# Performance work log

Measured on AMD Instinct MI355X. Metric: run time of the kernel, lower is better.

Reference implementation:

```python
import jax, jax.numpy as jnp
import numpy as np


def setup_inputs() -> dict:
    key = jax.random.key(0)
    k1, k2, k3 = jax.random.split(key, 3)
    B, C, H, W = 16, 256, 48, 48
    INTER = C // 2
    x = jax.random.normal(k1, (B, C, H, W), dtype=jnp.float32)
    # nn.init.normal_(weight, std=0.01); 1x1 conv kernels stored as (out, in)
    theta_w = 0.01 * jax.random.normal(k2, (INTER, C), dtype=jnp.float32)
    phi_w = 0.01 * jax.random.normal(k3, (INTER, C), dtype=jnp.float32)
    theta_b = jnp.zeros((INTER,), dtype=jnp.float32)
    phi_b = jnp.zeros((INTER,), dtype=jnp.float32)
    return {"x": x, "theta_w": theta_w, "theta_b": theta_b, "phi_w": phi_w, "phi_b": phi_b}


def reference(x, theta_w, theta_b, phi_w, phi_b):
    b, c, h, w = x.shape
    inter = theta_w.shape[0]
    n = h * w
    # 1x1 conv == channel-wise linear projection
    theta_x = jnp.einsum('bchw,kc->bkhw', x, theta_w) + theta_b[None, :, None, None]
    phi_x = jnp.einsum('bchw,kc->bkhw', x, phi_w) + phi_b[None, :, None, None]
    q = theta_x.reshape(b, inter, n)   # [b, k, n]
    kmat = phi_x.reshape(b, inter, n)  # [b, k, n]
    g = x.reshape(b, c, n)             # [b, c, n]
    # f = theta^T @ phi : [b, n, n], scaled then softmaxed over last dim
    f = jnp.einsum('bkn,bkm->bnm', q, kmat) / jnp.sqrt(jnp.asarray(inter, x.dtype))
    f = jax.nn.softmax(f, axis=-1)
    # y = f @ g^T : [b, c, n]
    y = jnp.einsum('bnm,bcm->bcn', f, g)
    return y.reshape(b, c, h, w)
```

## Files before the change

### kernel.cpp

```cpp
#include <hip/hip_runtime.h>
#include <hip/hip_bf16.h>

#define B_SZ 16
#define C_IN 256
#define N_SP 2304
#define K_INT 128
#define NTILE 36
#define MT 32
#define MITER 72

typedef __attribute__((ext_vector_type(8))) short short8;
typedef __attribute__((ext_vector_type(4))) float f32x4;

__device__ inline unsigned pk_bf16(float a, float b) {
  float2 f; f.x = a; f.y = b;
  __hip_bfloat162 h = __float22bfloat162_rn(f);
  unsigned u;
  __builtin_memcpy(&u, &h, sizeof(u));
  return u;
}

__device__ inline short8 ldw_bf16(const float* __restrict__ W, int k, int c0) {
  const float* wp = W + (size_t)k * C_IN + c0;
  float4 w0 = ((const float4*)wp)[0];
  float4 w1 = ((const float4*)wp)[1];
  unsigned u[4];
  u[0] = pk_bf16(w0.x, w0.y); u[1] = pk_bf16(w0.z, w0.w);
  u[2] = pk_bf16(w1.x, w1.y); u[3] = pk_bf16(w1.z, w1.w);
  short8 a;
  __builtin_memcpy(&a, u, sizeof(a));
  return a;
}

__global__ __launch_bounds__(256) void proj_kernel(
    const float* __restrict__ x,
    const float* __restrict__ theta_w, const float* __restrict__ theta_b,
    const float* __restrict__ phi_w,   const float* __restrict__ phi_b,
    short* __restrict__ Qt, short* __restrict__ Kt, short* __restrict__ Gbf)
{
  __shared__ __align__(16) char Xs[32768];

  const int b  = blockIdx.x / NTILE;
  const int n0 = (blockIdx.x % NTILE) * 64;
  const int t  = threadIdx.x;
  const int wave = t >> 6, lane = t & 63;
  const int col = lane & 15, quad = lane >> 4;

  {
    const int tq = t >> 4;
    const int a  = t & 15;
    const float* xs = x + ((size_t)b * C_IN + tq * 4) * N_SP + n0 + a * 4;
    short* gs = Gbf + ((size_t)b * C_IN + tq * 4) * N_SP + n0 + a * 4;
#pragma unroll
    for (int s = 0; s < 4; ++s) {
      unsigned us[4][2];
#pragma unroll
      for (int r = 0; r < 4; ++r) {
        float4 v = *(const float4*)(xs + ((size_t)s * 64 + r) * N_SP);
        us[r][0] = pk_bf16(v.x, v.y);
        us[r][1] = pk_bf16(v.z, v.w);
        uint2 u; u.x = us[r][0]; u.y = us[r][1];
        *(uint2*)(gs + ((size_t)s * 64 + r) * N_SP) = u;
      }
      const int chunk = 8 * s + (tq >> 1);
      const int half8 = (tq & 1) * 8;
#pragma unroll
      for (int j = 0; j < 4; ++j) {
        const int w = j >> 1;
        unsigned w0, w1;
        if ((j & 1) == 0) {
          w0 = (us[0][w] & 0xffffu) | (us[1][w] << 16);
          w1 = (us[2][w] & 0xffffu) | (us[3][w] << 16);
        } else {
          w0 = (us[0][w] >> 16) | (us[1][w] & 0xffff0000u);
          w1 = (us[2][w] >> 16) | (us[3][w] & 0xffff0000u);
        }
        const int n = 4 * a + j;
        const int msk = (n ^ a) & 7;
        uint2 u; u.x = w0; u.y = w1;
        *(uint2*)(Xs + n * 512 + ((chunk ^ msk) << 4) + half8) = u;
      }
    }
  }
  __syncthreads();

  f32x4 acc[2][2][4];
#pragma unroll
  for (int p = 0; p < 2; ++p)
#pragma unroll
    for (int kr = 0; kr < 2; ++kr)
#pragma unroll
      for (int j = 0; j < 4; ++j) {
        acc[p][kr][j][0] = 0.f; acc[p][kr][j][1] = 0.f;
        acc[p][kr][j][2] = 0.f; acc[p][kr][j][3] = 0.f;
      }

  int rmsk[4];
#pragma unroll
  for (int j = 0; j < 4; ++j) {
    const int n = 16 * j + col;
    rmsk[j] = (n ^ (n >> 2)) & 7;
  }

#pragma unroll
  for (int cs = 0; cs < 8; ++cs) {
    const int c0 = cs * 32;
    short8 afr[2][2];
#pragma unroll
    for (int p = 0; p < 2; ++p)
#pragma unroll
      for (int kr = 0; kr < 2; ++kr) {
        const int k = wave * 32 + kr * 16 + col;
        afr[p][kr] = ldw_bf16(p ? phi_w : theta_w, k, c0 + quad * 8);
      }
#pragma unroll
    for (int j = 0; j < 4; ++j) {
      const int chunk = 4 * cs + quad;
      short8 bfr = *(const short8*)(Xs + (16 * j + col) * 512 +
                                    ((chunk ^ rmsk[j]) << 4));
#pragma unroll
      for (int p = 0; p < 2; ++p)
#pragma unroll
        for (int kr = 0; kr < 2; ++kr)
          acc[p][kr][j] = __builtin_amdgcn_mfma_f32_16x16x32_bf16(
              afr[p][kr], bfr, acc[p][kr][j], 0, 0, 0);
    }
  }
  __syncthreads();

  short* PB = (short*)Xs;
#pragma unroll
  for (int p = 0; p < 2; ++p) {
    const float* bias = p ? phi_b : theta_b;
    short* dst0 = p ? Kt : Qt;
#pragma unroll
    for (int kr = 0; kr < 2; ++kr) {
      const int k0 = wave * 32 + kr * 16 + quad * 4;
      float4 bv = *(const float4*)(bias + k0);
      const int g = wave * 8 + kr * 4 + quad;
#pragma unroll
      for (int j = 0; j < 4; ++j) {
        const int nloc = j * 16 + col;
        f32x4 v = acc[p][kr][j];
        uint2 sv;
        sv.x = pk_bf16(v[0] + bv.x, v[1] + bv.y);
        sv.y = pk_bf16(v[2] + bv.z, v[3] + bv.w);
        const int gp = g ^ (nloc & 7) ^ (((nloc >> 3) & 1) << 3);
        *(uint2*)(PB + nloc * 128 + gp * 4) = sv;
      }
    }
    __syncthreads();
    {
      const int nloc = t >> 2, kseg = t & 3;
      const int xb = ((nloc >> 3) & 1) << 3;
      uint2 r8[8];
#pragma unroll
      for (int i = 0; i < 8; ++i) {
        const int gp = (kseg * 8 + i) ^ (nloc & 7) ^ xb;
        r8[i] = *(const uint2*)(PB + nloc * 128 + gp * 4);
      }
      short* dst = dst0 + ((size_t)b * N_SP + n0 + nloc) * K_INT + kseg * 32;
#pragma unroll
      for (int i2 = 0; i2 < 4; ++i2) {
        uint4 u;
        u.x = r8[2 * i2].x;     u.y = r8[2 * i2].y;
        u.z = r8[2 * i2 + 1].x; u.w = r8[2 * i2 + 1].y;
        *(uint4*)(dst + i2 * 8) = u;
      }
    }
    __syncthreads();
  }
}

__global__ __launch_bounds__(256) void attn_kernel(
    const short* __restrict__ Qt, const short* __restrict__ Kt,
    const short* __restrict__ Gbf, float* __restrict__ out)
{
  __shared__ __align__(16) char Kl[2][8192];
  __shared__ __align__(16) short Pblob[2][4][64][8];
  __shared__ float l_lds[64];

  const int b   = blockIdx.x / NTILE;
  const int qn0 = (blockIdx.x % NTILE) * 64;
  const int t = threadIdx.x;
  const int wave = t >> 6, lane = t & 63;
  const int col = lane & 15, quad = lane >> 4;

  const short* Ktb = Kt  + (size_t)b * N_SP * K_INT;
  const short* Gb  = Gbf + (size_t)b * C_IN * N_SP;

  short8 qf[4];
  {
    const short* qb = Qt + ((size_t)b * N_SP + qn0 + wave * 16 + col) * K_INT + quad * 8;
#pragma unroll
    for (int kk = 0; kk < 4; ++kk) qf[kk] = *(const short8*)(qb + kk * 32);
  }

  f32x4 yacc[4][4];
#pragma unroll
  for (int i = 0; i < 4; ++i)
#pragma unroll
    for (int j = 0; j < 4; ++j) {
      yacc[i][j][0] = 0.f; yacc[i][j][1] = 0.f;
      yacc[i][j][2] = 0.f; yacc[i][j][3] = 0.f;
    }
  f32x4 lacc;
  lacc[0] = 0.f; lacc[1] = 0.f; lacc[2] = 0.f; lacc[3] = 0.f;

  short8 ones;
#pragma unroll
  for (int j = 0; j < 8; ++j) ones[j] = (short)0x3F80;

  const float SC2 = 0.12754859f;

  const int KW = (t >> 4) * 256 + ((((t & 15) ^ ((t >> 4) & 7))) << 4);
  int KR0[4];
#pragma unroll
  for (int kk = 0; kk < 4; ++kk)
    KR0[kk] = col * 256 + ((((kk << 2) + quad) ^ (col & 7)) << 4);

  const int koff = (t >> 4) * K_INT + (t & 15) * 8;
  const short* gbase = Gb + ((size_t)(wave * 64 + col)) * N_SP + quad * 8;

  short8 krA, krB;
  krA = *(const short8*)(Ktb + koff);
  krB = *(const short8*)(Ktb + 2048 + koff);
  *(short8*)(Kl[0] + KW) = krA;
  *(short8*)(Kl[0] + KW + 4096) = krB;
  krA = *(const short8*)(Ktb + 4096 + koff);
  krB = *(const short8*)(Ktb + 6144 + koff);
  short8 gA[4], gB[4];
#pragma unroll
  for (int ct = 0; ct < 4; ++ct)
    gA[ct] = *(const short8*)(gbase + (size_t)ct * 16 * N_SP);
  __syncthreads();

#define SUBITER(MTV, CUR, GC, GN)                                              \
  {                                                                            \
                           \
    f32x4 s0, s1;                                                              \
    s0[0] = 0.f; s0[1] = 0.f; s0[2] = 0.f; s0[3] = 0.f;                        \
    s1[0] = 0.f; s1[1] = 0.f; s1[2] = 0.f; s1[3] = 0.f;                        \
    _Pragma("unroll")                                                          \
    for (int kk = 0; kk < 4; ++kk) {                                           \
      short8 a0 = *(const short8*)(Kl[CUR] + KR0[kk]);                         \
      s0 = __builtin_amdgcn_mfma_f32_16x16x32_bf16(a0, qf[kk], s0, 0, 0, 0);   \
      short8 a1 = *(const short8*)(Kl[CUR] + KR0[kk] + 4096);                  \
      s1 = __builtin_amdgcn_mfma_f32_16x16x32_bf16(a1, qf[kk], s1, 0, 0, 0);   \
    }                                                                          \
                    \
    unsigned u0 = pk_bf16(exp2f(s0[0] * SC2), exp2f(s0[1] * SC2));             \
    unsigned u1 = pk_bf16(exp2f(s0[2] * SC2), exp2f(s0[3] * SC2));             \
    unsigned u2 = pk_bf16(exp2f(s1[0] * SC2), exp2f(s1[1] * SC2));             \
    unsigned u3 = pk_bf16(exp2f(s1[2] * SC2), exp2f(s1[3] * SC2));             \
    asm("v_permlane32_swap_b32 %0, %1" : "+v"(u0), "+v"(u2));                  \
    asm("v_permlane32_swap_b32 %0, %1" : "+v"(u1), "+v"(u3));                  \
    asm("v_permlane16_swap_b32 %0, %1" : "+v"(u0), "+v"(u2));                  \
    asm("v_permlane16_swap_b32 %0, %1" : "+v"(u1), "+v"(u3));                  \
    unsigned uu[4] = {u0, u1, u2, u3};                                         \
    short8 pa; __builtin_memcpy(&pa, uu, 16);                                  \
    lacc = __builtin_amdgcn_mfma_f32_16x16x32_bf16(pa, ones, lacc, 0, 0, 0);   \
                         \
    *(short8*)&Pblob[CUR][wave][lane][0] = pa;                                 \
        \
    if ((MTV) + 1 < MITER) {                                                   \
      *(short8*)(Kl[(CUR) ^ 1] + KW) = krA;                                    \
      *(short8*)(Kl[(CUR) ^ 1] + KW + 4096) = krB;                             \
    }                                                                          \
                      \
    if ((MTV) + 2 < MITER) {                                                   \
      const short* kp = Ktb + (size_t)((MTV) + 2) * 4096 + koff;               \
      krA = *(const short8*)(kp);                                              \
      krB = *(const short8*)(kp + 2048);                                       \
    }                                                                          \
               \
    if ((MTV) + 1 < MITER) {                                                   \
      _Pragma("unroll")                                                        \
      for (int ct = 0; ct < 4; ++ct)                                           \
        GN[ct] = *(const short8*)(gbase + (size_t)ct * 16 * N_SP +             \
                                  ((MTV) + 1) * 32);                           \
    }                                                                          \
    __syncthreads();                                                           \
             \
    _Pragma("unroll")                                                          \
    for (int qt = 0; qt < 4; ++qt) {                                           \
      short8 paq = *(const short8*)&Pblob[CUR][qt][lane][0];                   \
      _Pragma("unroll")                                                        \
      for (int ct = 0; ct < 4; ++ct)                                           \
        yacc[qt][ct] = __builtin_amdgcn_mfma_f32_16x16x32_bf16(                \
            paq, GC[ct], yacc[qt][ct], 0, 0, 0);                               \
    }                                                                          \
  }

  for (int mt2 = 0; mt2 < MITER / 2; ++mt2) {
    SUBITER(2 * mt2,     0, gA, gB)
    SUBITER(2 * mt2 + 1, 1, gB, gA)
  }
#undef SUBITER

  if (col == 0) {
#pragma unroll
    for (int r = 0; r < 4; ++r) l_lds[wave * 16 + quad * 4 + r] = lacc[r];
  }
  __syncthreads();

#pragma unroll
  for (int qt = 0; qt < 4; ++qt) {
    float4 lq = *(const float4*)&l_lds[qt * 16 + quad * 4];
    float4 iv;
    iv.x = 1.0f / lq.x; iv.y = 1.0f / lq.y; iv.z = 1.0f / lq.z; iv.w = 1.0f / lq.w;
    const int nb = qn0 + qt * 16 + quad * 4;
#pragma unroll
    for (int ct = 0; ct < 4; ++ct) {
      const int c = wave * 64 + ct * 16 + col;
      f32x4 v = yacc[qt][ct];
      float4 o;
      o.x = v[0] * iv.x; o.y = v[1] * iv.y; o.z = v[2] * iv.z; o.w = v[3] * iv.w;
      *(float4*)(out + ((size_t)b * C_IN + c) * N_SP + nb) = o;
    }
  }
}

extern "C" void kernel_launch(void* const* d_in, const int* in_sizes, int n_in,
                              void* d_out, int out_size, void* d_ws, size_t ws_size,
                              hipStream_t stream) {
  const float* x  = (const float*)d_in[0];
  const float* tw = (const float*)d_in[1];
  const float* tb = (const float*)d_in[2];
  const float* pw = (const float*)d_in[3];
  const float* pb = (const float*)d_in[4];
  float* out = (float*)d_out;

  short* Qt  = (short*)d_ws;
  short* Kt  = Qt + (size_t)B_SZ * N_SP * K_INT;
  short* Gbf = Kt + (size_t)B_SZ * N_SP * K_INT;

  proj_kernel<<<B_SZ * NTILE, 256, 0, stream>>>(x, tw, tb, pw, pb, Qt, Kt, Gbf);
  attn_kernel<<<B_SZ * NTILE, 256, 0, stream>>>(Qt, Kt, Gbf, out);
}
```

Before: 247.3 us.

## Load K fragments directly from global into registers, bypassing LDS staging

Removes the shared-memory double buffer for K tiles; each wave now loads its MFMA A-operand fragments for the K tile straight from global memory into registers, prefetched one iteration ahead. This removes the LDS write/read traffic and the initial barrier for K. In exchange, every wave redundantly fetches the whole K tile, so L2/global traffic for K rises fourfold. Prefetch distance also drops from two iterations to one, and register usage grows.

New measurement: 404.5 us. +63.6%, slower.

```diff
diff --git a/kernel.cpp b/kernel.cpp
--- a/kernel.cpp
+++ b/kernel.cpp
@@ -176,7 +176,6 @@
     const short* __restrict__ Qt, const short* __restrict__ Kt,
     const short* __restrict__ Gbf, float* __restrict__ out)
 {
-  __shared__ __align__(16) char Kl[2][8192];
   __shared__ __align__(16) short Pblob[2][4][64][8];
   __shared__ float l_lds[64];
 
@@ -213,40 +212,42 @@
 
   const float SC2 = 0.12754859f;
 
-  const int KW = (t >> 4) * 256 + ((((t & 15) ^ ((t >> 4) & 7))) << 4);
-  int KR0[4];
-#pragma unroll
-  for (int kk = 0; kk < 4; ++kk)
-    KR0[kk] = col * 256 + ((((kk << 2) + quad) ^ (col & 7)) << 4);
-
-  const int koff = (t >> 4) * K_INT + (t & 15) * 8;
+  const short* kbase = Ktb + col * K_INT + quad * 8;
   const short* gbase = Gb + ((size_t)(wave * 64 + col)) * N_SP + quad * 8;
 
-  short8 krA, krB;
-  krA = *(const short8*)(Ktb + koff);
-  krB = *(const short8*)(Ktb + 2048 + koff);
-  *(short8*)(Kl[0] + KW) = krA;
-  *(short8*)(Kl[0] + KW + 4096) = krB;
-  krA = *(const short8*)(Ktb + 4096 + koff);
-  krB = *(const short8*)(Ktb + 6144 + koff);
+  short8 kf[8];
+#pragma unroll
+  for (int kk = 0; kk < 4; ++kk) {
+    kf[2 * kk]     = *(const short8*)(kbase + kk * 32);
+    kf[2 * kk + 1] = *(const short8*)(kbase + 2048 + kk * 32);
+  }
   short8 gA[4], gB[4];
 #pragma unroll
   for (int ct = 0; ct < 4; ++ct)
     gA[ct] = *(const short8*)(gbase + (size_t)ct * 16 * N_SP);
-  __syncthreads();
 
 #define SUBITER(MTV, CUR, GC, GN)                                              \
   {                                                                            \
-                           \
+                     \
     f32x4 s0, s1;                                                              \
     s0[0] = 0.f; s0[1] = 0.f; s0[2] = 0.f; s0[3] = 0.f;                        \
     s1[0] = 0.f; s1[1] = 0.f; s1[2] = 0.f; s1[3] = 0.f;                        \
     _Pragma("unroll")                                                          \
     for (int kk = 0; kk < 4; ++kk) {                                           \
-      short8 a0 = *(const short8*)(Kl[CUR] + KR0[kk]);                         \
-      s0 = __builtin_amdgcn_mfma_f32_16x16x32_bf16(a0, qf[kk], s0, 0, 0, 0);   \
-      short8 a1 = *(const short8*)(Kl[CUR] + KR0[kk] + 4096);                  \
-      s1 = __builtin_amdgcn_mfma_f32_16x16x32_bf16(a1, qf[kk], s1, 0, 0, 0);   \
+      s0 = __builtin_amdgcn_mfma_f32_16x16x32_bf16(kf[2 * kk],     qf[kk],     \
+                                                   s0, 0, 0, 0);               \
+      s1 = __builtin_amdgcn_mfma_f32_16x16x32_bf16(kf[2 * kk + 1], qf[kk],     \
+                                                   s1, 0, 0, 0);               \
+    }                                                                          \
+           \
+        \
+    if ((MTV) + 1 < MITER) {                                                   \
+      const short* kp = kbase + (size_t)((MTV) + 1) * 4096;                    \
+      _Pragma("unroll")                                                        \
+      for (int kk = 0; kk < 4; ++kk) {                                         \
+        kf[2 * kk]     = *(const short8*)(kp + kk * 32);                       \
+        kf[2 * kk + 1] = *(const short8*)(kp + 2048 + kk * 32);                \
+      }                                                                        \
     }                                                                          \
                     \
     unsigned u0 = pk_bf16(exp2f(s0[0] * SC2), exp2f(s0[1] * SC2));             \
@@ -262,17 +263,6 @@
     lacc = __builtin_amdgcn_mfma_f32_16x16x32_bf16(pa, ones, lacc, 0, 0, 0);   \
                          \
     *(short8*)&Pblob[CUR][wave][lane][0] = pa;                                 \
-        \
-    if ((MTV) + 1 < MITER) {                                                   \
-      *(short8*)(Kl[(CUR) ^ 1] + KW) = krA;                                    \
-      *(short8*)(Kl[(CUR) ^ 1] + KW + 4096) = krB;                             \
-    }                                                                          \
-                      \
-    if ((MTV) + 2 < MITER) {                                                   \
-      const short* kp = Ktb + (size_t)((MTV) + 2) * 4096 + koff;               \
-      krA = *(const short8*)(kp);                                              \
-      krB = *(const short8*)(kp + 2048);                                       \
-    }                                                                          \
                \
     if ((MTV) + 1 < MITER) {                                                   \
       _Pragma("unroll")                                                        \
```
